# Optimization experiments

Hardware: AMD Instinct MI355X
Metric: run time of the kernel (lower is better)

The kernel has to match this reference:

```python
import jax, jax.numpy as jnp
import numpy as np

B, SMAX, TMAX, D = 8, 4096, 4096, 528


def setup_inputs() -> dict:
    key = jax.random.key(0)
    ks = jax.random.split(key, 20)
    src_lens = (np.arange(B) * 256 + 2048).astype(np.int64)  # 2048..3840, sum 23552
    tgt_lens = (np.arange(B) * 224 + 2304).astype(np.int64)  # 2304..3872, sum 24704
    Ns, Nt = int(src_lens.sum()), int(tgt_lens.sum())
    N = Ns + Nt  # 48256 packed coarse points (src then tgt)
    src_mask = jnp.asarray(np.arange(SMAX)[None, :] < src_lens[:, None])
    tgt_mask = jnp.asarray(np.arange(TMAX)[None, :] < tgt_lens[:, None])
    sics = np.concatenate([b * SMAX + np.arange(l) for b, l in enumerate(src_lens)])
    tics = np.concatenate([b * TMAX + np.arange(l) for b, l in enumerate(tgt_lens)])
    w = lambda k, shape: (jax.random.normal(k, shape, jnp.float32) * 0.02)
    return dict(
        geo_feats=jax.random.normal(ks[0], (N, D), jnp.float32),
        pcd=jax.random.normal(ks[1], (N, 3), jnp.float32),
        Wi1=w(ks[2], (528, 528)), bi1=w(ks[3], (528,)),
        Wi2=w(ks[4], (1024, 528)), bi2=w(ks[5], (1024,)),
        Wc1=w(ks[6], (528, 528)), bc1=w(ks[7], (528,)),
        Wc2=w(ks[8], (1024, 528)), bc2=w(ks[9], (1024,)),
        Ws1=w(ks[10], (512, 2576)), bs1=w(ks[11], (512,)),
        Ws2=w(ks[12], (256, 512)), bs2=w(ks[13], (256,)),
        Ws3=w(ks[14], (1, 256)), bs3=w(ks[15], (1,)),
        src_mask=src_mask, tgt_mask=tgt_mask,
        src_ind_coarse_split=jnp.asarray(sics, jnp.int32),
        tgt_ind_coarse_split=jnp.asarray(tics, jnp.int32),
        src_ind_coarse=jnp.arange(Ns, dtype=jnp.int32),
        tgt_ind_coarse=Ns + jnp.arange(Nt, dtype=jnp.int32),
    )


def _scatter(vals, flat_idx, b, n, d):
    # split_feats: zeros[b*n, d]; out[flat_idx] = vals; view(b, n, d)
    return jnp.zeros((b * n, d), vals.dtype).at[flat_idx].set(vals).reshape(b, n, d)


def _pw(x, W, b):
    # pointwise Conv1d(in->out, k=1) as a batched matmul over positions
    return jnp.einsum('bnd,od->bno', x, W) + b


def reference(geo_feats, pcd, Wi1, bi1, Wi2, bi2, Wc1, bc1, Wc2, bc2,
              Ws1, bs1, Ws2, bs2, Ws3, bs3,
              src_mask, tgt_mask, src_ind_coarse_split, tgt_ind_coarse_split,
              src_ind_coarse, tgt_ind_coarse):
    b, smax = src_mask.shape
    tmax = tgt_mask.shape[1]
    d = geo_feats.shape[-1]

    # split_feats: ragged gather -> padded [B, pts_max, D]
    src_feats = _scatter(geo_feats[src_ind_coarse], src_ind_coarse_split, b, smax, d)
    tgt_feats = _scatter(geo_feats[tgt_ind_coarse], tgt_ind_coarse_split, b, tmax, d)
    s_pcd = _scatter(pcd[src_ind_coarse], src_ind_coarse_split, b, smax, 3)
    t_pcd = _scatter(pcd[tgt_ind_coarse], tgt_ind_coarse_split, b, tmax, 3)

    sm = src_mask.astype(src_feats.dtype)
    tm = tgt_mask.astype(tgt_feats.dtype)

    # inst_global over valid src points (per-sample slice -> masked mean)
    h = jax.nn.relu(_pw(src_feats, Wi1, bi1))
    h = jax.nn.relu(_pw(h, Wi2, bi2))                      # [B, Smax, 1024]
    inst_g = jnp.einsum('bno,bn->bo', h, sm) / sm.sum(1, keepdims=True)

    # category_global over valid tgt points
    g = jax.nn.relu(_pw(tgt_feats, Wc1, bc1))
    g = jax.nn.relu(_pw(g, Wc2, bc2))                      # [B, Tmax, 1024]
    cat_g = jnp.einsum('bno,bn->bo', g, tm) / tm.sum(1, keepdims=True)

    # scale_net on concat(src_feats, inst_g, cat_g) without materializing [B,N,2576]:
    # split first conv weight over the concat axis; globals contribute per-batch constants
    Ws1_s, Ws1_i, Ws1_c = Ws1[:, :d], Ws1[:, d:d + 1024], Ws1[:, d + 1024:]
    glob = inst_g @ Ws1_i.T + cat_g @ Ws1_c.T + bs1        # [B, 512]
    z = jax.nn.relu(jnp.einsum('bnd,od->bno', src_feats, Ws1_s) + glob[:, None, :])
    z = jax.nn.relu(_pw(z, Ws2, bs2))                      # [B, Smax, 256]
    s = _pw(z, Ws3, bs3)                                   # [B, Smax, 1]
    scale_mat = jax.nn.sigmoid(s).transpose(0, 2, 1) - 0.5  # [B, 1, Smax]

    inv = 1.0 / jnp.sqrt(jnp.asarray(d, src_feats.dtype))
    return (src_feats * inv, tgt_feats * inv, s_pcd, t_pcd, scale_mat)
```

## Files before the change

kernel.cpp:

```cpp
#include <hip/hip_runtime.h>
#include <hip/hip_bf16.h>
#include <cstdint>
#include <cstddef>

typedef float f32x4 __attribute__((ext_vector_type(4)));
typedef __bf16 bf16x8v __attribute__((ext_vector_type(8)));
typedef __hip_bfloat16 bf16;

__device__ __forceinline__ void gld16(const void* g, void* l) {
  __builtin_amdgcn_global_load_lds((const __attribute__((address_space(1))) void*)g,
                                   (__attribute__((address_space(3))) void*)l, 16, 0, 0);
}


struct PrepP {
  const float* Wsrc[6];
  bf16* Wdst[6];
  int sld[6], rows[6], K[6], Kpad[6];
  int off[10];
  float* zbuf; int ztotal;
  const float* geo; bf16* geo_b; int Nrows;
  const int* sics; const int* tics; int Ns, Nt; int* cnt;
};

__global__ void prep_kernel(PrepP P) {
  int blk = blockIdx.x;
  int job = 0;
  while (job < 8 && blk >= P.off[job + 1]) ++job;
  int local = blk - P.off[job];
  if (job < 6) {
    int i = local * 256 + threadIdx.x;
    int kp = P.Kpad[job];
    int total = P.rows[job] * kp;
    if (i < total) {
      int r = i / kp, k = i - r * kp;
      float v = (k < P.K[job]) ? P.Wsrc[job][(size_t)r * P.sld[job] + k] : 0.f;
      P.Wdst[job][i] = __float2bfloat16(v);
    }
  } else if (job == 6) {
    int i = local * 256 + threadIdx.x;
    if (i < P.ztotal) P.zbuf[i] = 0.f;
  } else if (job == 7) {
    int t = local * 256 + threadIdx.x;
    int row = t / 72, c8 = t - row * 72;
    if (row < P.Nrows) {
      int col = c8 * 8;
      bf16* dst = P.geo_b + (size_t)row * 576 + col;
      if (c8 < 66) {
        const float* s = P.geo + (size_t)row * 528 + col;
        float4 f0 = ((const float4*)s)[0], f1 = ((const float4*)s)[1];
        bf16 h[8] = {__float2bfloat16(f0.x), __float2bfloat16(f0.y),
                     __float2bfloat16(f0.z), __float2bfloat16(f0.w),
                     __float2bfloat16(f1.x), __float2bfloat16(f1.y),
                     __float2bfloat16(f1.z), __float2bfloat16(f1.w)};
        ((uint4*)dst)[0] = *(uint4*)h;
      } else {
        uint4 z = {0u, 0u, 0u, 0u};
        ((uint4*)dst)[0] = z;
      }
    }
  } else {
    int j = local * 256 + threadIdx.x;
    if (j < P.Ns) {
      if (j == 0) { P.cnt[0] = 0; P.cnt[8] = P.Ns; }
      else { int b = P.sics[j] >> 12; if ((P.sics[j - 1] >> 12) != b) P.cnt[b] = j; }
    }
    if (j < P.Nt) {
      if (j == 0) { P.cnt[9] = 0; P.cnt[17] = P.Nt; }
      else { int b = P.tics[j] >> 12; if ((P.tics[j - 1] >> 12) != b) P.cnt[9 + b] = j; }
    }
  }
}

__device__ __forceinline__ void gemm_core(
    const bf16* __restrict__ Aptr, int lda,
    const bf16* __restrict__ Bw, int ldb,
    int m0, int n0, int kiters,
    bf16* __restrict__ lA, bf16* __restrict__ lB,
    f32x4 acc[4][4])
{
  const int tid  = threadIdx.x;
  const int lane = tid & 63;
  const int quad = lane >> 4;
  const int l16  = lane & 15;
  const int wr   = tid >> 7;
  const int wc   = (tid >> 6) & 1;
  const int srow = tid >> 2;
  const int scol = (tid & 3) << 3;
  const bf16* aA0 = Aptr + (size_t)(m0 + srow) * lda + scol;
  const bf16* aA1 = aA0 + (size_t)64 * lda;
  const bf16* aB0 = Bw + (size_t)(n0 + srow) * ldb + scol;
  const bf16* aB1 = aB0 + (size_t)64 * ldb;
  bf16* lA00 = lA + tid * 8;        bf16* lA01 = lA + 2048 + tid * 8;
  bf16* lA10 = lA + 4096 + tid * 8; bf16* lA11 = lA + 6144 + tid * 8;
  bf16* lB00 = lB + tid * 8;        bf16* lB01 = lB + 2048 + tid * 8;
  bf16* lB10 = lB + 4096 + tid * 8; bf16* lB11 = lB + 6144 + tid * 8;

  for (int k = 0; k < kiters; ++k) {
    const int k0 = k * 64;
    gld16(aA0 + k0, lA00);      gld16(aA1 + k0, lA01);
    gld16(aA0 + k0 + 32, lA10); gld16(aA1 + k0 + 32, lA11);
    gld16(aB0 + k0, lB00);      gld16(aB1 + k0, lB01);
    gld16(aB0 + k0 + 32, lB10); gld16(aB1 + k0 + 32, lB11);
    __syncthreads();
#pragma unroll
    for (int kk = 0; kk < 2; ++kk) {
      bf16x8v af[4], bfr[4];
#pragma unroll
      for (int i = 0; i < 4; ++i) {
        af[i]  = *(const bf16x8v*)&lA[kk * 4096 + (wr * 64 + i * 16 + l16) * 32 + quad * 8];
        bfr[i] = *(const bf16x8v*)&lB[kk * 4096 + (wc * 64 + i * 16 + l16) * 32 + quad * 8];
      }
#pragma unroll
      for (int mi = 0; mi < 4; ++mi)
#pragma unroll
        for (int ni = 0; ni < 4; ++ni)
          acc[mi][ni] = __builtin_amdgcn_mfma_f32_16x16x32_bf16(af[mi], bfr[ni], acc[mi][ni], 0, 0, 0);
    }
    __syncthreads();
  }
}

__global__ __launch_bounds__(256, 2)
void kernelA(const bf16* __restrict__ geo_b,
             const bf16* __restrict__ Wi1b, const bf16* __restrict__ Wc1b,
             const bf16* __restrict__ Ws1sb,
             const float* __restrict__ bi1, const float* __restrict__ bc1,
             bf16* __restrict__ big_s, bf16* __restrict__ big_t,
             bf16* __restrict__ zpre, int Ms, int Mt)
{
  __shared__ alignas(16) bf16 lA[8192], lB[8192];
  const int x = blockIdx.x;
  const int e0 = Ms * 5, e1 = e0 + Mt * 5;
  const bf16 *A, *B; const float* bias = nullptr; bf16* out;
  int m0, n0, ldo, epi;
  if (x < e0) {
    int mt = x / 5, nt = x - mt * 5;
    m0 = mt * 128; n0 = nt * 128;
    A = geo_b; B = Wi1b; bias = bi1; out = big_s; ldo = 576; epi = 0;
  } else if (x < e1) {
    int y = x - e0; int mt = y / 5, nt = y - mt * 5;
    m0 = mt * 128; n0 = nt * 128;
    A = geo_b + (size_t)Ms * 128 * 576; B = Wc1b; bias = bc1; out = big_t; ldo = 576; epi = 0;
  } else {
    int y = x - e1; int mt = y / 4, nt = y - mt * 4;
    m0 = mt * 128; n0 = nt * 128;
    A = geo_b; B = Ws1sb; out = zpre; ldo = 512; epi = 1;
  }

  f32x4 acc[4][4];
  const f32x4 z4 = {0.f, 0.f, 0.f, 0.f};
#pragma unroll
  for (int i = 0; i < 4; ++i)
#pragma unroll
    for (int j = 0; j < 4; ++j) acc[i][j] = z4;

  gemm_core(A, 576, B, 576, m0, n0, 9, lA, lB, acc);

  const int lane = threadIdx.x & 63, quad = lane >> 4, l16 = lane & 15;
  const int wr = threadIdx.x >> 7, wc = (threadIdx.x >> 6) & 1;
#pragma unroll
  for (int mi = 0; mi < 4; ++mi) {
#pragma unroll
    for (int r = 0; r < 4; ++r) {
      const int row = m0 + wr * 64 + mi * 16 + quad * 4 + r;
#pragma unroll
      for (int ni = 0; ni < 4; ++ni) {
        const int col = n0 + wc * 64 + ni * 16 + l16;
        if (epi == 0) {
          if (col < 528)
            out[(size_t)row * ldo + col] = __float2bfloat16(fmaxf(acc[mi][ni][r] + bias[col], 0.f));
          else if (col < 576)
            out[(size_t)row * ldo + col] = __float2bfloat16(0.f);
        } else {
          out[(size_t)row * ldo + col] = __float2bfloat16(acc[mi][ni][r]);
        }
      }
    }
  }
}

__global__ __launch_bounds__(256, 2)
void kernelB(const bf16* __restrict__ big_s, const bf16* __restrict__ big_t,
             const bf16* __restrict__ Wi2b, const bf16* __restrict__ Wc2b,
             const float* __restrict__ bi2, const float* __restrict__ bc2,
             float* __restrict__ iacc, float* __restrict__ cacc,
             const int* __restrict__ sics, const int* __restrict__ tics,
             int Ms, int Mt,
             const float* __restrict__ geo, const float* __restrict__ pcd,
             const int* __restrict__ cnt,
             float* __restrict__ out0, float* __restrict__ out1,
             float* __restrict__ out2, float* __restrict__ out3,
             int Ns, float inv)
{
  __shared__ alignas(16) bf16 lA[8192], lB[8192];
  const int x = blockIdx.x;
  const int e0 = Ms * 8, e1 = e0 + Mt * 8;
  if (x >= e1) {
    int f = x - e1;
    int lane = threadIdx.x & 63;
    int rv = f * 4 + (threadIdx.x >> 6);
    bool is_t = rv >= 32768;
    int pos = is_t ? rv - 32768 : rv;
    int b = pos >> 12, r = pos & 4095;
    int base = is_t ? cnt[9 + b] : cnt[b];
    int lim  = (is_t ? cnt[9 + b + 1] : cnt[b + 1]) - base;
    float* op = (is_t ? out1 : out0) + (size_t)pos * 528;
    float* pp = (is_t ? out3 : out2) + (size_t)pos * 3;
    if (r < lim) {
      int sr = (is_t ? Ns : 0) + base + r;
      const float4* g = (const float4*)(geo + (size_t)sr * 528);
      for (int d = lane; d < 132; d += 64) {
        float4 v = g[d];
        float4 s = {v.x * inv, v.y * inv, v.z * inv, v.w * inv};
        ((float4*)op)[d] = s;
      }
      if (lane < 3) pp[lane] = pcd[(size_t)sr * 3 + lane];
    } else {
      float4 z = {0.f, 0.f, 0.f, 0.f};
      for (int d = lane; d < 132; d += 64) ((float4*)op)[d] = z;
      if (lane < 3) pp[lane] = 0.f;
    }
    return;
  }
  const bf16 *A, *B; const float* bias; float* red; const int* ridx;
  int m0, n0;
  if (x < e0) {
    int mt = x / 8, nt = x - mt * 8;
    m0 = mt * 128; n0 = nt * 128;
    A = big_s; B = Wi2b; bias = bi2; red = iacc; ridx = sics;
  } else {
    int y = x - e0; int mt = y / 8, nt = y - mt * 8;
    m0 = mt * 128; n0 = nt * 128;
    A = big_t; B = Wc2b; bias = bc2; red = cacc; ridx = tics;
  }

  f32x4 acc[4][4];
  const f32x4 z4 = {0.f, 0.f, 0.f, 0.f};
#pragma unroll
  for (int i = 0; i < 4; ++i)
#pragma unroll
    for (int j = 0; j < 4; ++j) acc[i][j] = z4;

  gemm_core(A, 576, B, 576, m0, n0, 9, lA, lB, acc);

  const int lane = threadIdx.x & 63, quad = lane >> 4, l16 = lane & 15;
  const int wr = threadIdx.x >> 7, wc = (threadIdx.x >> 6) & 1;
  const int b0r = ridx[m0] >> 12;
#pragma unroll
  for (int ni = 0; ni < 4; ++ni) {
    const int col = n0 + wc * 64 + ni * 16 + l16;
    const float bcol = bias[col];
#pragma unroll
    for (int mi = 0; mi < 4; ++mi) {
      float v0 = 0.f, v1 = 0.f;
#pragma unroll
      for (int r = 0; r < 4; ++r) {
        const int row = m0 + wr * 64 + mi * 16 + quad * 4 + r;
        const float v = fmaxf(acc[mi][ni][r] + bcol, 0.f);
        const int b = ridx[row] >> 12;
        if (b == b0r) v0 += v; else v1 += v;
      }
      v0 += __shfl_xor(v0, 16, 64); v0 += __shfl_xor(v0, 32, 64);
      v1 += __shfl_xor(v1, 16, 64); v1 += __shfl_xor(v1, 32, 64);
      if (quad == 0) {
        atomicAdd(&red[b0r * 1024 + col], v0);
        if (b0r + 1 < 8 && v1 != 0.f) atomicAdd(&red[(b0r + 1) * 1024 + col], v1);
      }
    }
  }
}

__global__ __launch_bounds__(256, 2)
void kernelC(const bf16* __restrict__ zpre, const bf16* __restrict__ Ws2b,
             const float* __restrict__ bs2, const float* __restrict__ Ws3,
             float* __restrict__ sbuf)
{
  __shared__ alignas(16) bf16 lA[8192], lB[8192];
  const int m0 = blockIdx.x * 128, n0 = blockIdx.y * 128;
  f32x4 acc[4][4];
  const f32x4 z4 = {0.f, 0.f, 0.f, 0.f};
#pragma unroll
  for (int i = 0; i < 4; ++i)
#pragma unroll
    for (int j = 0; j < 4; ++j) acc[i][j] = z4;

  gemm_core(zpre, 512, Ws2b, 512, m0, n0, 8, lA, lB, acc);

  const int lane = threadIdx.x & 63, quad = lane >> 4, l16 = lane & 15;
  const int wr = threadIdx.x >> 7, wc = (threadIdx.x >> 6) & 1;
#pragma unroll
  for (int mi = 0; mi < 4; ++mi) {
#pragma unroll
    for (int r = 0; r < 4; ++r) {
      const int row = m0 + wr * 64 + mi * 16 + quad * 4 + r;
      float p = 0.f;
#pragma unroll
      for (int ni = 0; ni < 4; ++ni) {
        const int col = n0 + wc * 64 + ni * 16 + l16;
        p += fmaxf(acc[mi][ni][r] + bs2[col], 0.f) * Ws3[col];
      }
      p += __shfl_xor(p, 1, 64); p += __shfl_xor(p, 2, 64);
      p += __shfl_xor(p, 4, 64); p += __shfl_xor(p, 8, 64);
      if (l16 == 0) atomicAdd(&sbuf[row], p);
    }
  }
}

__global__ __launch_bounds__(256) void glob_kernel(const float* __restrict__ iacc,
                                                   const float* __restrict__ cacc,
                                                   const int* __restrict__ cnt,
                                                   const float* __restrict__ Ws1,
                                                   const float* __restrict__ bs1,
                                                   float* __restrict__ globv) {
  int w    = (blockIdx.x * 256 + threadIdx.x) >> 6;
  int lane = threadIdx.x & 63;
  int b = w >> 9;
  int o = w & 511;
  const float* wi  = Ws1 + (size_t)o * 2576 + 528;
  const float* wcp = Ws1 + (size_t)o * 2576 + 1552;
  float a1 = 0.f, a2 = 0.f;
  for (int k = lane; k < 1024; k += 64) {
    a1 += iacc[b * 1024 + k] * wi[k];
    a2 += cacc[b * 1024 + k] * wcp[k];
  }
  for (int off = 32; off; off >>= 1) {
    a1 += __shfl_xor(a1, off, 64);
    a2 += __shfl_xor(a2, off, 64);
  }
  if (lane == 0) {
    float ns = (float)(cnt[b + 1] - cnt[b]);
    float nt = (float)(cnt[9 + b + 1] - cnt[9 + b]);
    globv[b * 512 + o] = bs1[o] + a1 / ns + a2 / nt;
  }
}

__global__ __launch_bounds__(256) void s_empty_kernel(const float* __restrict__ globv,
                                                      const float* __restrict__ Ws2,
                                                      const float* __restrict__ bs2,
                                                      const float* __restrict__ Ws3,
                                                      const float* __restrict__ bs3,
                                                      float* __restrict__ semp) {
  __shared__ float zrow[512];
  __shared__ float wsum[4];
  int b = blockIdx.x, t = threadIdx.x;
  zrow[t]       = fmaxf(globv[b * 512 + t], 0.f);
  zrow[t + 256] = fmaxf(globv[b * 512 + t + 256], 0.f);
  __syncthreads();
  float acc = bs2[t];
  for (int o = 0; o < 512; ++o) acc += zrow[o] * Ws2[t * 512 + o];
  float p = fmaxf(acc, 0.f) * Ws3[t];
  for (int off = 32; off; off >>= 1) p += __shfl_xor(p, off, 64);
  if ((t & 63) == 0) wsum[t >> 6] = p;
  __syncthreads();
  if (t == 0) semp[b] = wsum[0] + wsum[1] + wsum[2] + wsum[3] + bs3[0];
}

__global__ void zfix_kernel(bf16* __restrict__ z, const float* __restrict__ globv,
                            const int* __restrict__ sics, int total) {
  int idx = blockIdx.x * 256 + threadIdx.x;
  if (idx >= total) return;
  int row = idx >> 6, c0 = (idx & 63) << 3;
  int b = sics[row] >> 12;
  const float* gv = globv + b * 512 + c0;
  bf16* zp = z + (size_t)row * 512 + c0;
  uint4 u = *(uint4*)zp;
  bf16* e = (bf16*)&u;
#pragma unroll
  for (int i = 0; i < 8; ++i)
    e[i] = __float2bfloat16(fmaxf(__bfloat162float(e[i]) + gv[i], 0.f));
  *(uint4*)zp = u;
}

__global__ void scale_kernel(const float* __restrict__ sbuf,
                             const float* __restrict__ semp,
                             const int* __restrict__ cnt,
                             const float* __restrict__ bs3,
                             float* __restrict__ out4) {
  int i = blockIdx.x * 256 + threadIdx.x;
  if (i >= 32768) return;
  int b = i >> 12, r = i & 4095;
  int base = cnt[b];
  int lim = cnt[b + 1] - base;
  float s = (r < lim) ? sbuf[base + r] + bs3[0] : semp[b];
  out4[i] = 1.f / (1.f + expf(-s)) - 0.5f;
}


extern "C" void kernel_launch(void* const* d_in, const int* in_sizes, int n_in,
                              void* d_out, int out_size, void* d_ws, size_t ws_size,
                              hipStream_t stream) {
  const float* geo = (const float*)d_in[0];
  const float* pcd = (const float*)d_in[1];
  const float* Wi1 = (const float*)d_in[2];
  const float* bi1 = (const float*)d_in[3];
  const float* Wi2 = (const float*)d_in[4];
  const float* bi2 = (const float*)d_in[5];
  const float* Wc1 = (const float*)d_in[6];
  const float* bc1 = (const float*)d_in[7];
  const float* Wc2 = (const float*)d_in[8];
  const float* bc2 = (const float*)d_in[9];
  const float* Ws1 = (const float*)d_in[10];
  const float* bs1 = (const float*)d_in[11];
  const float* Ws2 = (const float*)d_in[12];
  const float* bs2 = (const float*)d_in[13];
  const float* Ws3 = (const float*)d_in[14];
  const float* bs3 = (const float*)d_in[15];
  const int* sics = (const int*)d_in[18];
  const int* tics = (const int*)d_in[19];
  const int Ns = in_sizes[18];
  const int Nt = in_sizes[19];
  const int Ms = Ns / 128, Mt = Nt / 128;
  const int Nrows = Ns + Nt;

  float* out0 = (float*)d_out;
  float* out1 = out0 + (size_t)8 * 4096 * 528;
  float* out2 = out1 + (size_t)8 * 4096 * 528;
  float* out3 = out2 + (size_t)8 * 4096 * 3;
  float* out4 = out3 + (size_t)8 * 4096 * 3;

  char* wp = (char*)d_ws;
  auto alloc = [&](size_t bytes) -> void* {
    void* p = (void*)wp;
    wp += (bytes + 255) & ~(size_t)255;
    return p;
  };
  int*   cnt   = (int*)  alloc(128);
  float* iacc  = (float*)alloc((size_t)8 * 1024 * 4);
  float* cacc  = (float*)alloc((size_t)8 * 1024 * 4);
  float* sbuf  = (float*)alloc((size_t)Ns * 4);
  float* globb = (float*)alloc((size_t)8 * 512 * 4);
  float* semp  = (float*)alloc(64);
  bf16* Wi1b  = (bf16*)alloc((size_t)640  * 576 * 2);
  bf16* Wi2b  = (bf16*)alloc((size_t)1024 * 576 * 2);
  bf16* Wc1b  = (bf16*)alloc((size_t)640  * 576 * 2);
  bf16* Wc2b  = (bf16*)alloc((size_t)1024 * 576 * 2);
  bf16* Ws1sb = (bf16*)alloc((size_t)512  * 576 * 2);
  bf16* Ws2b  = (bf16*)alloc((size_t)256  * 512 * 2);
  bf16* geo_b = (bf16*)alloc((size_t)Nrows * 576 * 2);
  bf16* big_s = (bf16*)alloc((size_t)Ns * 576 * 2);
  bf16* big_t = (bf16*)alloc((size_t)Nt * 576 * 2);
  bf16* zpre  = (bf16*)alloc((size_t)Ns * 512 * 2);

  PrepP P;
  {
    const float* srcs[6] = {Wi1, Wi2, Wc1, Wc2, Ws1, Ws2};
    bf16* dsts[6]        = {Wi1b, Wi2b, Wc1b, Wc2b, Ws1sb, Ws2b};
    int slds[6] = {528, 528, 528, 528, 2576, 512};
    int rows[6] = {528, 1024, 528, 1024, 512, 256};
    int Ks[6]   = {528, 528, 528, 528, 528, 512};
    int Kps[6]  = {576, 576, 576, 576, 576, 512};
    int nblk = 0;
    for (int i = 0; i < 6; ++i) {
      P.Wsrc[i] = srcs[i]; P.Wdst[i] = dsts[i]; P.sld[i] = slds[i];
      P.rows[i] = rows[i]; P.K[i] = Ks[i]; P.Kpad[i] = Kps[i];
      P.off[i] = nblk;
      nblk += (rows[i] * Kps[i] + 255) / 256;
    }
    P.off[6] = nblk;
    P.zbuf = iacc; P.ztotal = 8192 + 8192 + Ns;
    nblk += (P.ztotal + 255) / 256;
    P.off[7] = nblk;
    P.geo = geo; P.geo_b = geo_b; P.Nrows = Nrows;
    nblk += ((Nrows * 72) + 255) / 256;
    P.off[8] = nblk;
    P.sics = sics; P.tics = tics; P.Ns = Ns; P.Nt = Nt; P.cnt = cnt;
    int n = Ns > Nt ? Ns : Nt;
    nblk += (n + 255) / 256;
    P.off[9] = nblk;
    prep_kernel<<<dim3(nblk), dim3(256), 0, stream>>>(P);
  }

  kernelA<<<dim3(Ms * 5 + Mt * 5 + Ms * 4), dim3(256), 0, stream>>>(
      geo_b, Wi1b, Wc1b, Ws1sb, bi1, bc1, big_s, big_t, zpre, Ms, Mt);

  float inv = 1.0f / sqrtf(528.0f);
  kernelB<<<dim3(Ms * 8 + Mt * 8 + 16384), dim3(256), 0, stream>>>(
      big_s, big_t, Wi2b, Wc2b, bi2, bc2, iacc, cacc, sics, tics, Ms, Mt,
      geo, pcd, cnt, out0, out1, out2, out3, Ns, inv);

  glob_kernel<<<dim3(1024), dim3(256), 0, stream>>>(iacc, cacc, cnt, Ws1, bs1, globb);
  s_empty_kernel<<<dim3(8), dim3(256), 0, stream>>>(globb, Ws2, bs2, Ws3, bs3, semp);
  zfix_kernel<<<dim3((Ns * 64 + 255) / 256), dim3(256), 0, stream>>>(zpre, globb, sics, Ns * 64);
  kernelC<<<dim3(Ms, 2), dim3(256), 0, stream>>>(zpre, Ws2b, bs2, Ws3, sbuf);
  scale_kernel<<<dim3(128), dim3(256), 0, stream>>>(sbuf, semp, cnt, bs3, out4);
}
```

Measured before the change: 518.2 us.

## Widen kernelB GEMM tile to 128x256 and coalesce s_empty weight reads

kernelB's second-layer GEMM now gives each block a 128x256 output tile instead of 128x128. The tile loop is inlined with direct global-to-LDS loads and twice the MFMA accumulators per wave, so each A tile is loaded once for twice as many columns and block count and atomics per row tile are halved. s_empty_kernel switches from one thread per output row reading strided weights to wave-cooperative dot products with coalesced Ws2 reads. The wider tile doubles accumulator registers and LDS per block, which risks spilling or lower occupancy under launch_bounds(256,2).

```diff
diff --git a/kernel.cpp b/kernel.cpp
--- a/kernel.cpp
+++ b/kernel.cpp
@@ -193,9 +193,9 @@
              float* __restrict__ out2, float* __restrict__ out3,
              int Ns, float inv)
 {
-  __shared__ alignas(16) bf16 lA[8192], lB[8192];
+  __shared__ alignas(16) bf16 lA[8192], lB[16384];
   const int x = blockIdx.x;
-  const int e0 = Ms * 8, e1 = e0 + Mt * 8;
+  const int e0 = Ms * 4, e1 = e0 + Mt * 4;
   if (x >= e1) {
     int f = x - e1;
     int lane = threadIdx.x & 63;
@@ -226,46 +226,87 @@
   const bf16 *A, *B; const float* bias; float* red; const int* ridx;
   int m0, n0;
   if (x < e0) {
-    int mt = x / 8, nt = x - mt * 8;
-    m0 = mt * 128; n0 = nt * 128;
+    int mt = x >> 2, g = x & 3;
+    m0 = mt * 128; n0 = g * 256;
     A = big_s; B = Wi2b; bias = bi2; red = iacc; ridx = sics;
   } else {
-    int y = x - e0; int mt = y / 8, nt = y - mt * 8;
-    m0 = mt * 128; n0 = nt * 128;
+    int y = x - e0; int mt = y >> 2, g = y & 3;
+    m0 = mt * 128; n0 = g * 256;
     A = big_t; B = Wc2b; bias = bc2; red = cacc; ridx = tics;
   }
 
-  f32x4 acc[4][4];
+  const int tid  = threadIdx.x;
+  const int lane = tid & 63, quad = lane >> 4, l16 = lane & 15;
+  const int wr = tid >> 7, wc = (tid >> 6) & 1;
+  const int srow = tid >> 2;
+  const int scol = (tid & 3) << 3;
+  const bf16* aA0 = A + (size_t)(m0 + srow) * 576 + scol;
+  const bf16* aA1 = aA0 + (size_t)64 * 576;
+  const bf16* aB0 = B + (size_t)(n0 + srow) * 576 + scol;
+  const bf16* aB1 = aB0 + (size_t)64 * 576;
+  const bf16* aB2 = aB0 + (size_t)128 * 576;
+  const bf16* aB3 = aB0 + (size_t)192 * 576;
+
+  f32x4 acc[4][8];
   const f32x4 z4 = {0.f, 0.f, 0.f, 0.f};
 #pragma unroll
   for (int i = 0; i < 4; ++i)
 #pragma unroll
-    for (int j = 0; j < 4; ++j) acc[i][j] = z4;
-
-  gemm_core(A, 576, B, 576, m0, n0, 9, lA, lB, acc);
-
-  const int lane = threadIdx.x & 63, quad = lane >> 4, l16 = lane & 15;
-  const int wr = threadIdx.x >> 7, wc = (threadIdx.x >> 6) & 1;
+    for (int j = 0; j < 8; ++j) acc[i][j] = z4;
+
+  for (int k = 0; k < 9; ++k) {
+    const int k0 = k * 64;
+    gld16(aA0 + k0, lA + tid * 8);           gld16(aA1 + k0, lA + 2048 + tid * 8);
+    gld16(aA0 + k0 + 32, lA + 4096 + tid * 8); gld16(aA1 + k0 + 32, lA + 6144 + tid * 8);
+    gld16(aB0 + k0, lB + tid * 8);           gld16(aB1 + k0, lB + 2048 + tid * 8);
+    gld16(aB0 + k0 + 32, lB + 4096 + tid * 8); gld16(aB1 + k0 + 32, lB + 6144 + tid * 8);
+    gld16(aB2 + k0, lB + 8192 + tid * 8);    gld16(aB3 + k0, lB + 10240 + tid * 8);
+    gld16(aB2 + k0 + 32, lB + 12288 + tid * 8); gld16(aB3 + k0 + 32, lB + 14336 + tid * 8);
+    __syncthreads();
+#pragma unroll
+    for (int kk = 0; kk < 2; ++kk) {
+      bf16x8v af[4], bf0[4], bf1[4];
+#pragma unroll
+      for (int i = 0; i < 4; ++i) {
+        const int ro = (wc * 64 + i * 16 + l16) * 32 + quad * 8;
+        af[i]  = *(const bf16x8v*)&lA[kk * 4096 + (wr * 64 + i * 16 + l16) * 32 + quad * 8];
+        bf0[i] = *(const bf16x8v*)&lB[kk * 4096 + ro];
+        bf1[i] = *(const bf16x8v*)&lB[8192 + kk * 4096 + ro];
+      }
+#pragma unroll
+      for (int mi = 0; mi < 4; ++mi)
+#pragma unroll
+        for (int ni = 0; ni < 4; ++ni) {
+          acc[mi][ni]     = __builtin_amdgcn_mfma_f32_16x16x32_bf16(af[mi], bf0[ni], acc[mi][ni], 0, 0, 0);
+          acc[mi][4 + ni] = __builtin_amdgcn_mfma_f32_16x16x32_bf16(af[mi], bf1[ni], acc[mi][4 + ni], 0, 0, 0);
+        }
+    }
+    __syncthreads();
+  }
+
   const int b0r = ridx[m0] >> 12;
 #pragma unroll
-  for (int ni = 0; ni < 4; ++ni) {
-    const int col = n0 + wc * 64 + ni * 16 + l16;
-    const float bcol = bias[col];
-#pragma unroll
-    for (int mi = 0; mi < 4; ++mi) {
-      float v0 = 0.f, v1 = 0.f;
-#pragma unroll
-      for (int r = 0; r < 4; ++r) {
-        const int row = m0 + wr * 64 + mi * 16 + quad * 4 + r;
-        const float v = fmaxf(acc[mi][ni][r] + bcol, 0.f);
-        const int b = ridx[row] >> 12;
-        if (b == b0r) v0 += v; else v1 += v;
-      }
-      v0 += __shfl_xor(v0, 16, 64); v0 += __shfl_xor(v0, 32, 64);
-      v1 += __shfl_xor(v1, 16, 64); v1 += __shfl_xor(v1, 32, 64);
-      if (quad == 0) {
-        atomicAdd(&red[b0r * 1024 + col], v0);
-        if (b0r + 1 < 8 && v1 != 0.f) atomicAdd(&red[(b0r + 1) * 1024 + col], v1);
+  for (int t = 0; t < 2; ++t) {
+#pragma unroll
+    for (int ni = 0; ni < 4; ++ni) {
+      const int col = n0 + t * 128 + wc * 64 + ni * 16 + l16;
+      const float bcol = bias[col];
+#pragma unroll
+      for (int mi = 0; mi < 4; ++mi) {
+        float v0 = 0.f, v1 = 0.f;
+#pragma unroll
+        for (int r = 0; r < 4; ++r) {
+          const int row = m0 + wr * 64 + mi * 16 + quad * 4 + r;
+          const float v = fmaxf(acc[mi][t * 4 + ni][r] + bcol, 0.f);
+          const int b = ridx[row] >> 12;
+          if (b == b0r) v0 += v; else v1 += v;
+        }
+        v0 += __shfl_xor(v0, 16, 64); v0 += __shfl_xor(v0, 32, 64);
+        v1 += __shfl_xor(v1, 16, 64); v1 += __shfl_xor(v1, 32, 64);
+        if (quad == 0) {
+          atomicAdd(&red[b0r * 1024 + col], v0);
+          if (b0r + 1 < 8 && v1 != 0.f) atomicAdd(&red[(b0r + 1) * 1024 + col], v1);
+        }
       }
     }
   }
@@ -347,11 +388,19 @@
   zrow[t]       = fmaxf(globv[b * 512 + t], 0.f);
   zrow[t + 256] = fmaxf(globv[b * 512 + t + 256], 0.f);
   __syncthreads();
-  float acc = bs2[t];
-  for (int o = 0; o < 512; ++o) acc += zrow[o] * Ws2[t * 512 + o];
-  float p = fmaxf(acc, 0.f) * Ws3[t];
-  for (int off = 32; off; off >>= 1) p += __shfl_xor(p, off, 64);
-  if ((t & 63) == 0) wsum[t >> 6] = p;
+  int w = t >> 6, lane = t & 63;
+  float ws = 0.f;
+  for (int tt = w * 64; tt < w * 64 + 64; ++tt) {
+    float a = 0.f;
+#pragma unroll
+    for (int oi = 0; oi < 8; ++oi) {
+      int o = lane + oi * 64;
+      a += zrow[o] * Ws2[(size_t)tt * 512 + o];
+    }
+    for (int off = 32; off; off >>= 1) a += __shfl_xor(a, off, 64);
+    if (lane == 0) ws += fmaxf(a + bs2[tt], 0.f) * Ws3[tt];
+  }
+  if (lane == 0) wsum[w] = ws;
   __syncthreads();
   if (t == 0) semp[b] = wsum[0] + wsum[1] + wsum[2] + wsum[3] + bs3[0];
 }
@@ -475,7 +524,7 @@
       geo_b, Wi1b, Wc1b, Ws1sb, bi1, bc1, big_s, big_t, zpre, Ms, Mt);
 
   float inv = 1.0f / sqrtf(528.0f);
-  kernelB<<<dim3(Ms * 8 + Mt * 8 + 16384), dim3(256), 0, stream>>>(
+  kernelB<<<dim3(Ms * 4 + Mt * 4 + 16384), dim3(256), 0, stream>>>(
       big_s, big_t, Wi2b, Wc2b, bi2, bc2, iacc, cacc, sics, tics, Ms, Mt,
       geo, pcd, cnt, out0, out1, out2, out3, Ns, inv);
 
```

After: 580.7 us. 1.12x slower.
